# Optimization experiments

Measured on AMD Instinct MI355X. Metric: run time of the kernel, lower is better.

The kernel has to match this reference:

```python
import jax, jax.numpy as jnp
import numpy as np

DIM = 1024
HEADS = 16
HIDDEN = int(DIM * 4.0)


def setup_inputs() -> dict:
    key = jax.random.key(0)
    ks = jax.random.split(key, 12)
    s = 0.02
    return {
        "x": jax.random.normal(ks[0], (16, 1024, DIM), dtype=jnp.float32),
        "ln1_g": jnp.ones((DIM,), jnp.float32),
        "ln1_b": jnp.zeros((DIM,), jnp.float32),
        "w_qkv": jax.random.normal(ks[1], (DIM, 3 * DIM), jnp.float32) * s,
        "b_qkv": jnp.zeros((3 * DIM,), jnp.float32),
        "w_proj": jax.random.normal(ks[2], (DIM, DIM), jnp.float32) * s,
        "b_proj": jnp.zeros((DIM,), jnp.float32),
        "ln2_g": jnp.ones((DIM,), jnp.float32),
        "ln2_b": jnp.zeros((DIM,), jnp.float32),
        "w_fc1": jax.random.normal(ks[3], (DIM, HIDDEN), jnp.float32) * s,
        "b_fc1": jnp.zeros((HIDDEN,), jnp.float32),
        "w_fc2": jax.random.normal(ks[4], (HIDDEN, DIM), jnp.float32) * s,
        "b_fc2": jnp.zeros((DIM,), jnp.float32),
    }


def _layernorm(x, g, b, eps=1e-5):
    mu = jnp.mean(x, axis=-1, keepdims=True)
    var = jnp.var(x, axis=-1, keepdims=True)
    return (x - mu) * jax.lax.rsqrt(var + eps) * g + b


def reference(x, ln1_g, ln1_b, w_qkv, b_qkv, w_proj, b_proj,
              ln2_g, ln2_b, w_fc1, b_fc1, w_fc2, b_fc2):
    B, N, C = x.shape
    H = HEADS
    hd = C // H
    scale = hd ** -0.5

    h = _layernorm(x, ln1_g, ln1_b)
    qkv = h @ w_qkv + b_qkv                      # [B,N,3C]
    qkv = qkv.reshape(B, N, 3, H, hd).transpose(2, 0, 3, 1, 4)
    q, k, v = qkv[0], qkv[1], qkv[2]             # [B,H,N,hd]

    attn = jnp.einsum("bhqd,bhkd->bhqk", q, k) * scale
    # original does explicit max-subtract then softmax; identical to stable softmax
    attn = jax.nn.softmax(attn, axis=-1)
    ctx = jnp.einsum("bhqk,bhkd->bhqd", attn, v)  # [B,H,N,hd]
    ctx = ctx.transpose(0, 2, 1, 3).reshape(B, N, C)
    attn_out = ctx @ w_proj + b_proj

    x = x + attn_out
    h2 = _layernorm(x, ln2_g, ln2_b)
    m = jax.nn.gelu(h2 @ w_fc1 + b_fc1, approximate=False)
    m = m @ w_fc2 + b_fc2
    return x + m
```

## Files before the change

### kernel.cpp

```cpp
#include <hip/hip_runtime.h>
#include <hip/hip_bf16.h>
#include <math.h>

using v8s   = __attribute__((ext_vector_type(8))) short;
using f32x4 = __attribute__((ext_vector_type(4))) float;

#define DEV __device__ __forceinline__

DEV void gload16(const void* g, void* l) {
  __builtin_amdgcn_global_load_lds(
      (const __attribute__((address_space(1))) unsigned int*)g,
      (__attribute__((address_space(3))) unsigned int*)l,
      16, 0, 0);
}

__global__ __launch_bounds__(256) void transpose_cast(
    const float* __restrict__ in, __hip_bfloat16* __restrict__ out, int K, int N)
{
  __shared__ float tile[32][33];
  const int n0 = blockIdx.x * 32, k0 = blockIdx.y * 32;
  const int tx = threadIdx.x, ty = threadIdx.y;
#pragma unroll
  for (int j = 0; j < 4; ++j)
    tile[ty + j*8][tx] = in[(size_t)(k0 + ty + j*8) * N + n0 + tx];
  __syncthreads();
#pragma unroll
  for (int j = 0; j < 4; ++j)
    out[(size_t)(n0 + ty + j*8) * K + k0 + tx] = __float2bfloat16(tile[tx][ty + j*8]);
}

__global__ __launch_bounds__(256) void ln_kernel(
    const float* __restrict__ xin, const float* __restrict__ g,
    const float* __restrict__ b, __hip_bfloat16* __restrict__ outp)
{
  const int row = blockIdx.x;
  const int t = threadIdx.x;
  const float4 v = ((const float4*)(xin + (size_t)row * 1024))[t];
  float s  = v.x + v.y + v.z + v.w;
  float ss = v.x*v.x + v.y*v.y + v.z*v.z + v.w*v.w;
  for (int off = 32; off > 0; off >>= 1) { s += __shfl_down(s, off); ss += __shfl_down(ss, off); }
  __shared__ float red[8];
  const int w = t >> 6;
  if ((t & 63) == 0) { red[w*2] = s; red[w*2 + 1] = ss; }
  __syncthreads();
  s  = red[0] + red[2] + red[4] + red[6];
  ss = red[1] + red[3] + red[5] + red[7];
  const float mu   = s * (1.0f / 1024.0f);
  const float rstd = rsqrtf(ss * (1.0f / 1024.0f) - mu * mu + 1e-5f);
  const float4 gv = ((const float4*)g)[t];
  const float4 bv = ((const float4*)b)[t];
  __hip_bfloat16* o = outp + (size_t)row * 1024 + t * 4;
  o[0] = __float2bfloat16((v.x - mu) * rstd * gv.x + bv.x);
  o[1] = __float2bfloat16((v.y - mu) * rstd * gv.y + bv.y);
  o[2] = __float2bfloat16((v.z - mu) * rstd * gv.z + bv.z);
  o[3] = __float2bfloat16((v.w - mu) * rstd * gv.w + bv.w);
}

#define STAGE_A(tile, ks, buf) do { int tt_ = (tile) < NT ? (tile) : NT - 1;     \
  _Pragma("unroll") for (int rr_ = 0; rr_ < 2; ++rr_) {                          \
    const int c_ = rr_*512 + t; const int row_ = c_ >> 2; const int sl_ = c_ & 3;\
    const int sw_ = sl_ ^ ((row_ >> 1) & 3);                                     \
    gload16(A + (size_t)(bm0 + row_) * K + tt_*64 + (ks)*32 + sw_*8,             \
            &As[buf][ks][row_][sl_*8]); } } while (0)

#define STAGE_B(tile, ks, buf) do { int tt_ = (tile) < NT ? (tile) : NT - 1;     \
  _Pragma("unroll") for (int rr_ = 0; rr_ < 2; ++rr_) {                          \
    const int c_ = rr_*512 + t; const int row_ = c_ >> 2; const int sl_ = c_ & 3;\
    const int sw_ = sl_ ^ ((row_ >> 1) & 3);                                     \
    gload16(Bt + (size_t)(bn0 + row_) * K + tt_*64 + (ks)*32 + sw_*8,            \
            &Bs[buf][ks][row_][sl_*8]); } } while (0)

#define LDB4(dst, c, ks) do { _Pragma("unroll") for (int n_ = 0; n_ < 4; ++n_) { \
  const int row_ = bwrow + n_*16;                                                \
  dst[n_] = *(const v8s*)&Bs[c][ks][row_][(lg ^ ((row_>>1)&3))*8]; } } while (0)

#define LDA4(dst, c, ks, mh) do { _Pragma("unroll") for (int m_ = 0; m_ < 4; ++m_) { \
  const int row_ = awrow + (mh)*64 + m_*16;                                      \
  dst[m_] = *(const v8s*)&As[c][ks][row_][(lg ^ ((row_>>1)&3))*8]; } } while (0)

#define MFMA16(av, bv, mh) do {                                                  \
  __builtin_amdgcn_s_setprio(1);                                                 \
  _Pragma("unroll") for (int mi_ = 0; mi_ < 4; ++mi_)                            \
    _Pragma("unroll") for (int n_ = 0; n_ < 4; ++n_)                             \
      acc[(mh)*4 + mi_][n_] = __builtin_amdgcn_mfma_f32_16x16x32_bf16(           \
          av[mi_], bv[n_], acc[(mh)*4 + mi_][n_], 0, 0, 0);                      \
  __builtin_amdgcn_s_setprio(0); } while (0)

template<int EPI>
__global__ __launch_bounds__(512, 2) void gemm256(
    const __hip_bfloat16* __restrict__ A, const __hip_bfloat16* __restrict__ Bt,
    const float* __restrict__ bias, const float* resid, void* outp,
    __hip_bfloat16* __restrict__ vt, int N, int K, int nbx)
{
  __shared__ __hip_bfloat16 As[2][2][256][32];
  __shared__ __hip_bfloat16 Bs[2][2][256][32];

  const int t = threadIdx.x;
  const int w = t >> 6, l = t & 63;
  const int wm = w >> 2, wn = w & 3;
  const int lr = l & 15, lg = l >> 4;
  const int awrow = wm * 128 + lr;
  const int bwrow = wn * 64 + lr;

  const int cpx  = gridDim.x >> 3;
  const int xcd  = blockIdx.x & 7;
  const int lid  = blockIdx.x >> 3;
  const int nbyc = cpx / nbx;
  const int span = nbyc * 4;
  const int gx   = lid / span;
  const int rem  = lid - gx * span;
  const int by   = xcd * nbyc + (rem >> 2);
  const int bx   = gx * 4 + (rem & 3);
  const size_t bm0 = (size_t)by * 256, bn0 = (size_t)bx * 256;

  const int NT = K >> 6;

  const f32x4 zz = {0.f, 0.f, 0.f, 0.f};
  f32x4 acc[8][4];
#pragma unroll
  for (int i = 0; i < 8; ++i)
#pragma unroll
    for (int j = 0; j < 4; ++j) acc[i][j] = zz;

  STAGE_A(0, 0, 0); STAGE_B(0, 0, 0);
  STAGE_A(0, 1, 0); STAGE_B(0, 1, 0);
  asm volatile("s_waitcnt vmcnt(0)" ::: "memory");
  __builtin_amdgcn_s_barrier();

  for (int tt = 0; tt < NT; ++tt) {
    const int c = tt & 1;
    v8s b0[4], a0[4], a1[4], b1[4], a2[4], a3[4];
    LDB4(b0, c, 0); LDA4(a0, c, 0, 0); LDA4(a1, c, 0, 1);
    LDB4(b1, c, 1); LDA4(a2, c, 1, 0); LDA4(a3, c, 1, 1);
    STAGE_A(tt + 1, 0, c ^ 1); STAGE_B(tt + 1, 0, c ^ 1);
    STAGE_A(tt + 1, 1, c ^ 1); STAGE_B(tt + 1, 1, c ^ 1);
    asm volatile("s_waitcnt lgkmcnt(12)" ::: "memory");
    __builtin_amdgcn_sched_barrier(0);
    MFMA16(a0, b0, 0);
    MFMA16(a1, b0, 1);
    asm volatile("s_waitcnt lgkmcnt(0)" ::: "memory");
    __builtin_amdgcn_sched_barrier(0);
    MFMA16(a2, b1, 0);
    MFMA16(a3, b1, 1);
    asm volatile("s_waitcnt vmcnt(0)" ::: "memory");
    __builtin_amdgcn_s_barrier();
  }

#pragma unroll
  for (int m = 0; m < 8; ++m)
#pragma unroll
    for (int n = 0; n < 4; ++n) {
      const int col = (int)bn0 + wn * 64 + n * 16 + lr;
      const float bz = bias[col];
#pragma unroll
      for (int r = 0; r < 4; ++r) {
        const int row = (int)bm0 + wm * 128 + m * 16 + lg * 4 + r;
        const float v = acc[m][n][r] + bz;
        if (EPI == 1) {
          ((float*)outp)[(size_t)row * N + col] = v + resid[(size_t)row * N + col];
        } else if (EPI == 2) {
          const float gel = 0.5f * v * (1.0f + erff(v * 0.70710678118654752f));
          ((__hip_bfloat16*)outp)[(size_t)row * N + col] = __float2bfloat16(gel);
        } else {
          if (col < 2048) {
            const float vv = (col < 1024) ? v * 0.18033688011112042f : v;
            ((__hip_bfloat16*)outp)[(size_t)row * 3072 + col] = __float2bfloat16(vv);
          } else {
            const int d = col - 2048;
            const int hh = d >> 6, dd = d & 63;
            const int bbq = row >> 10, nn = row & 1023;
            const int nnp = (nn & ~31) | (((nn & 15) << 1) | ((nn >> 4) & 1));
            vt[(((size_t)bbq * 16 + hh) * 64 + dd) * 1024 + nnp] = __float2bfloat16(v);
          }
        }
      }
    }
}

__global__ __launch_bounds__(512) void attn_kernel(
    const __hip_bfloat16* __restrict__ qkv, const __hip_bfloat16* __restrict__ vt,
    __hip_bfloat16* __restrict__ ctx)
{
  __shared__ __hip_bfloat16 Ks[2][64 * 64];
  __shared__ __hip_bfloat16 Vs[2][64 * 64];
  __shared__ __hip_bfloat16 Ps[8][32][72];

  const int t = threadIdx.x;
  const int w = t >> 6, l = t & 63;
  const int lr = l & 15, lg = l >> 4;

  const int lin  = blockIdx.x;
  const int xcd  = lin & 7;
  const int slot = lin >> 3;
  const int head = xcd * 32 + (slot >> 2);
  const int q0   = (slot & 3) * 256;
  const int bb = head >> 4, h = head & 15;
  const int tok0 = bb * 1024;
  const int qrow_base = tok0 + q0 + w * 32;

  const int srow0 = t >> 3, ssl0 = t & 7, ssw0 = ssl0 ^ (srow0 & 7);

  v8s qf[2][2];
#pragma unroll
  for (int i = 0; i < 2; ++i)
#pragma unroll
    for (int k2 = 0; k2 < 2; ++k2)
      qf[i][k2] = *(const v8s*)(qkv + (size_t)(qrow_base + i * 16 + lr) * 3072 + h * 64 + k2 * 32 + lg * 8);

  v8s vone;
#pragma unroll
  for (int e = 0; e < 8; ++e) vone[e] = (short)0x3F80;

  const f32x4 zz = {0.f, 0.f, 0.f, 0.f};
  f32x4 oacc[2][5];
#pragma unroll
  for (int i = 0; i < 2; ++i)
#pragma unroll
    for (int dg = 0; dg < 5; ++dg) oacc[i][dg] = zz;

  {
    gload16(qkv + (size_t)(tok0 + srow0) * 3072 + 1024 + h * 64 + ssw0 * 8, &Ks[0][t * 8]);
    gload16(vt  + (size_t)(head * 64 + srow0) * 1024 + ssw0 * 8,            &Vs[0][t * 8]);
  }
  asm volatile("s_waitcnt vmcnt(0)" ::: "memory");
  __builtin_amdgcn_s_barrier();

  for (int kt = 0; kt < 16; ++kt) {
    const int cur = kt & 1;
    if (kt < 15) {
      const int nxt = cur ^ 1;
      const int kn = (kt + 1) * 64;
      gload16(qkv + (size_t)(tok0 + kn + srow0) * 3072 + 1024 + h * 64 + ssw0 * 8, &Ks[nxt][t * 8]);
      gload16(vt  + (size_t)(head * 64 + srow0) * 1024 + kn + ssw0 * 8,            &Vs[nxt][t * 8]);
    }

    f32x4 s[2][4];
#pragma unroll
    for (int i = 0; i < 2; ++i)
#pragma unroll
      for (int j = 0; j < 4; ++j) s[i][j] = zz;
#pragma unroll
    for (int k2 = 0; k2 < 2; ++k2) {
      v8s kb[4];
#pragma unroll
      for (int j = 0; j < 4; ++j) {
        const int row = j * 16 + lr;
        kb[j] = *(const v8s*)(&Ks[cur][row * 64 + (((k2 * 4 + lg) ^ (row & 7)) * 8)]);
      }
#pragma unroll
      for (int i = 0; i < 2; ++i)
#pragma unroll
        for (int j = 0; j < 4; ++j)
          s[i][j] = __builtin_amdgcn_mfma_f32_16x16x32_bf16(qf[i][k2], kb[j], s[i][j], 0, 0, 0);
    }

#pragma unroll
    for (int i = 0; i < 2; ++i)
#pragma unroll
      for (int jj = 0; jj < 2; ++jj)
#pragma unroll
        for (int r = 0; r < 4; ++r) {
          const float lo = exp2f(s[i][2*jj][r]);
          const float hi = exp2f(s[i][2*jj + 1][r]);
          unsigned int pk;
          asm("v_cvt_pk_bf16_f32 %0, %1, %2" : "=v"(pk) : "v"(lo), "v"(hi));
          *(unsigned int*)&Ps[w][i * 16 + lg * 4 + r][jj * 32 + lr * 2] = pk;
        }

#pragma unroll
    for (int k2 = 0; k2 < 2; ++k2) {
      v8s pa[2];
#pragma unroll
      for (int i = 0; i < 2; ++i)
        pa[i] = *(const v8s*)&Ps[w][i * 16 + lr][k2 * 32 + lg * 8];
#pragma unroll
      for (int dg = 0; dg < 4; ++dg) {
        const int row = dg * 16 + lr;
        v8s vb = *(const v8s*)(&Vs[cur][row * 64 + (((k2 * 4 + lg) ^ (row & 7)) * 8)]);
#pragma unroll
        for (int i = 0; i < 2; ++i)
          oacc[i][dg] = __builtin_amdgcn_mfma_f32_16x16x32_bf16(pa[i], vb, oacc[i][dg], 0, 0, 0);
      }
#pragma unroll
      for (int i = 0; i < 2; ++i)
        oacc[i][4] = __builtin_amdgcn_mfma_f32_16x16x32_bf16(pa[i], vone, oacc[i][4], 0, 0, 0);
    }

    asm volatile("s_waitcnt vmcnt(0)" ::: "memory");
    __builtin_amdgcn_s_barrier();
  }

#pragma unroll
  for (int i = 0; i < 2; ++i) {
    float inv[4];
#pragma unroll
    for (int r = 0; r < 4; ++r) inv[r] = 1.0f / oacc[i][4][r];
#pragma unroll
    for (int dg = 0; dg < 4; ++dg)
#pragma unroll
      for (int r = 0; r < 4; ++r) {
        const int qrow = qrow_base + i * 16 + lg * 4 + r;
        ctx[(size_t)qrow * 1024 + h * 64 + dg * 16 + lr] = __float2bfloat16(oacc[i][dg][r] * inv[r]);
      }
  }
}

extern "C" void kernel_launch(void* const* d_in, const int* in_sizes, int n_in,
                              void* d_out, int out_size, void* d_ws, size_t ws_size,
                              hipStream_t stream) {
  const float* x      = (const float*)d_in[0];
  const float* ln1_g  = (const float*)d_in[1];
  const float* ln1_b  = (const float*)d_in[2];
  const float* w_qkv  = (const float*)d_in[3];
  const float* b_qkv  = (const float*)d_in[4];
  const float* w_proj = (const float*)d_in[5];
  const float* b_proj = (const float*)d_in[6];
  const float* ln2_g  = (const float*)d_in[7];
  const float* ln2_b  = (const float*)d_in[8];
  const float* w_fc1  = (const float*)d_in[9];
  const float* b_fc1  = (const float*)d_in[10];
  const float* w_fc2  = (const float*)d_in[11];
  const float* b_fc2  = (const float*)d_in[12];
  float* out = (float*)d_out;

  char* ws = (char*)d_ws;
  size_t off = 0;
  auto alloc = [&](size_t bytes) { char* p = ws + off; off += bytes; return p; };
  __hip_bfloat16* wqkvt  = (__hip_bfloat16*)alloc((size_t)3072 * 1024 * 2);
  __hip_bfloat16* wprojt = (__hip_bfloat16*)alloc((size_t)1024 * 1024 * 2);
  __hip_bfloat16* wfc1t  = (__hip_bfloat16*)alloc((size_t)4096 * 1024 * 2);
  __hip_bfloat16* wfc2t  = (__hip_bfloat16*)alloc((size_t)1024 * 4096 * 2);
  __hip_bfloat16* h      = (__hip_bfloat16*)alloc((size_t)16384 * 1024 * 2);
  __hip_bfloat16* qkvb   = (__hip_bfloat16*)alloc((size_t)16384 * 3072 * 2);
  __hip_bfloat16* vt     = (__hip_bfloat16*)alloc((size_t)256 * 64 * 1024 * 2);
  __hip_bfloat16* ctx    = (__hip_bfloat16*)alloc((size_t)16384 * 1024 * 2);
  __hip_bfloat16* mbuf   = qkvb;

  transpose_cast<<<dim3(3072/32, 1024/32), dim3(32, 8), 0, stream>>>(w_qkv,  wqkvt,  1024, 3072);
  transpose_cast<<<dim3(1024/32, 1024/32), dim3(32, 8), 0, stream>>>(w_proj, wprojt, 1024, 1024);
  transpose_cast<<<dim3(4096/32, 1024/32), dim3(32, 8), 0, stream>>>(w_fc1,  wfc1t,  1024, 4096);
  transpose_cast<<<dim3(1024/32, 4096/32), dim3(32, 8), 0, stream>>>(w_fc2,  wfc2t,  4096, 1024);

  ln_kernel<<<16384, 256, 0, stream>>>(x, ln1_g, ln1_b, h);
  gemm256<3><<<12 * 64, 512, 0, stream>>>(h,    wqkvt,  b_qkv,  nullptr, qkvb,  vt,      3072, 1024, 12);
  attn_kernel<<<1024, 512, 0, stream>>>(qkvb, vt, ctx);
  gemm256<1><<< 4 * 64, 512, 0, stream>>>(ctx,  wprojt, b_proj, x,       d_out, nullptr, 1024, 1024, 4);
  ln_kernel<<<16384, 256, 0, stream>>>(out, ln2_g, ln2_b, h);
  gemm256<2><<<16 * 64, 512, 0, stream>>>(h,    wfc1t,  b_fc1,  nullptr, mbuf,  nullptr, 4096, 1024, 16);
  gemm256<1><<< 4 * 64, 512, 0, stream>>>(mbuf, wfc2t,  b_fc2,  out,     d_out, nullptr, 1024, 4096, 4);
}
```

Baseline: 773.9 us.

## Replace 256x256 double-buffered GEMM with single-buffered 128x128 tile kernel

Swaps the 512-thread, 256x256-tile, double-buffered GEMM for a 256-thread 128x128-tile kernel with a single LDS buffer per operand, a 64-wide K step, an 8-way XOR swizzle, and a new supertile block mapping across XCDs. Smaller tiles give more blocks (4 per CU by launch bounds) and may improve occupancy and load balance on the small-N projections. In exchange it drops the overlap of global loads with MFMA (load then wait each iteration) and lowers arithmetic intensity per tile, which raises global/L2 traffic.

```diff
diff --git a/kernel.cpp b/kernel.cpp
--- a/kernel.cpp
+++ b/kernel.cpp
@@ -56,105 +56,91 @@
   o[3] = __float2bfloat16((v.w - mu) * rstd * gv.w + bv.w);
 }
 
-#define STAGE_A(tile, ks, buf) do { int tt_ = (tile) < NT ? (tile) : NT - 1;     \
-  _Pragma("unroll") for (int rr_ = 0; rr_ < 2; ++rr_) {                          \
-    const int c_ = rr_*512 + t; const int row_ = c_ >> 2; const int sl_ = c_ & 3;\
-    const int sw_ = sl_ ^ ((row_ >> 1) & 3);                                     \
-    gload16(A + (size_t)(bm0 + row_) * K + tt_*64 + (ks)*32 + sw_*8,             \
-            &As[buf][ks][row_][sl_*8]); } } while (0)
-
-#define STAGE_B(tile, ks, buf) do { int tt_ = (tile) < NT ? (tile) : NT - 1;     \
-  _Pragma("unroll") for (int rr_ = 0; rr_ < 2; ++rr_) {                          \
-    const int c_ = rr_*512 + t; const int row_ = c_ >> 2; const int sl_ = c_ & 3;\
-    const int sw_ = sl_ ^ ((row_ >> 1) & 3);                                     \
-    gload16(Bt + (size_t)(bn0 + row_) * K + tt_*64 + (ks)*32 + sw_*8,            \
-            &Bs[buf][ks][row_][sl_*8]); } } while (0)
-
-#define LDB4(dst, c, ks) do { _Pragma("unroll") for (int n_ = 0; n_ < 4; ++n_) { \
-  const int row_ = bwrow + n_*16;                                                \
-  dst[n_] = *(const v8s*)&Bs[c][ks][row_][(lg ^ ((row_>>1)&3))*8]; } } while (0)
-
-#define LDA4(dst, c, ks, mh) do { _Pragma("unroll") for (int m_ = 0; m_ < 4; ++m_) { \
-  const int row_ = awrow + (mh)*64 + m_*16;                                      \
-  dst[m_] = *(const v8s*)&As[c][ks][row_][(lg ^ ((row_>>1)&3))*8]; } } while (0)
-
-#define MFMA16(av, bv, mh) do {                                                  \
-  __builtin_amdgcn_s_setprio(1);                                                 \
-  _Pragma("unroll") for (int mi_ = 0; mi_ < 4; ++mi_)                            \
-    _Pragma("unroll") for (int n_ = 0; n_ < 4; ++n_)                             \
-      acc[(mh)*4 + mi_][n_] = __builtin_amdgcn_mfma_f32_16x16x32_bf16(           \
-          av[mi_], bv[n_], acc[(mh)*4 + mi_][n_], 0, 0, 0);                      \
-  __builtin_amdgcn_s_setprio(0); } while (0)
+
+#define STAGE_T(tile) do { const int tt_ = (tile);                               \
+  _Pragma("unroll") for (int rr_ = 0; rr_ < 4; ++rr_) {                          \
+    const int c_ = rr_*256 + t; const int row_ = c_ >> 3; const int sl_ = c_ & 7;\
+    const int sw_ = sl_ ^ (row_ & 7);                                            \
+    gload16(A + (size_t)(bm0 + row_) * K + tt_*64 + sw_*8, &As[row_][sl_*8]); }  \
+  _Pragma("unroll") for (int rr_ = 0; rr_ < 4; ++rr_) {                          \
+    const int c_ = rr_*256 + t; const int row_ = c_ >> 3; const int sl_ = c_ & 7;\
+    const int sw_ = sl_ ^ (row_ & 7);                                            \
+    gload16(Bt + (size_t)(bn0 + row_) * K + tt_*64 + sw_*8, &Bs[row_][sl_*8]); } } while (0)
+
+#define LDAB(k2) do {                                                            \
+  _Pragma("unroll") for (int mi_ = 0; mi_ < 4; ++mi_) {                          \
+    const int r_ = wm*64 + mi_*16 + lr;                                          \
+    a_[mi_] = *(const v8s*)&As[r_][((((k2)*4)+lg) ^ (r_ & 7))*8]; }              \
+  _Pragma("unroll") for (int ni_ = 0; ni_ < 4; ++ni_) {                          \
+    const int r_ = wn*64 + ni_*16 + lr;                                          \
+    b_[ni_] = *(const v8s*)&Bs[r_][((((k2)*4)+lg) ^ (r_ & 7))*8]; } } while (0)
 
 template<int EPI>
-__global__ __launch_bounds__(512, 2) void gemm256(
+__global__ __launch_bounds__(256, 4) void gemm128(
     const __hip_bfloat16* __restrict__ A, const __hip_bfloat16* __restrict__ Bt,
     const float* __restrict__ bias, const float* resid, void* outp,
     __hip_bfloat16* __restrict__ vt, int N, int K, int nbx)
 {
-  __shared__ __hip_bfloat16 As[2][2][256][32];
-  __shared__ __hip_bfloat16 Bs[2][2][256][32];
+  __shared__ __hip_bfloat16 As[128][64];
+  __shared__ __hip_bfloat16 Bs[128][64];
 
   const int t = threadIdx.x;
   const int w = t >> 6, l = t & 63;
-  const int wm = w >> 2, wn = w & 3;
+  const int wm = w >> 1, wn = w & 1;
   const int lr = l & 15, lg = l >> 4;
-  const int awrow = wm * 128 + lr;
-  const int bwrow = wn * 64 + lr;
-
-  const int cpx  = gridDim.x >> 3;
+
   const int xcd  = blockIdx.x & 7;
   const int lid  = blockIdx.x >> 3;
-  const int nbyc = cpx / nbx;
-  const int span = nbyc * 4;
-  const int gx   = lid / span;
-  const int rem  = lid - gx * span;
-  const int by   = xcd * nbyc + (rem >> 2);
-  const int bx   = gx * 4 + (rem & 3);
-  const size_t bm0 = (size_t)by * 256, bn0 = (size_t)bx * 256;
+  const int super = lid >> 5;
+  const int rem   = lid & 31;
+  const int nsx   = nbx >> 2;
+  const int gy    = super / nsx;
+  const int gx    = super - gy * nsx;
+  const int by    = xcd * 16 + gy * 8 + (rem >> 2);
+  const int bx    = gx * 4 + (rem & 3);
+  const size_t bm0 = (size_t)by * 128, bn0 = (size_t)bx * 128;
 
   const int NT = K >> 6;
 
   const f32x4 zz = {0.f, 0.f, 0.f, 0.f};
-  f32x4 acc[8][4];
-#pragma unroll
-  for (int i = 0; i < 8; ++i)
+  f32x4 acc[4][4];
+#pragma unroll
+  for (int i = 0; i < 4; ++i)
 #pragma unroll
     for (int j = 0; j < 4; ++j) acc[i][j] = zz;
 
-  STAGE_A(0, 0, 0); STAGE_B(0, 0, 0);
-  STAGE_A(0, 1, 0); STAGE_B(0, 1, 0);
-  asm volatile("s_waitcnt vmcnt(0)" ::: "memory");
-  __builtin_amdgcn_s_barrier();
-
+  v8s a_[4], b_[4];
   for (int tt = 0; tt < NT; ++tt) {
-    const int c = tt & 1;
-    v8s b0[4], a0[4], a1[4], b1[4], a2[4], a3[4];
-    LDB4(b0, c, 0); LDA4(a0, c, 0, 0); LDA4(a1, c, 0, 1);
-    LDB4(b1, c, 1); LDA4(a2, c, 1, 0); LDA4(a3, c, 1, 1);
-    STAGE_A(tt + 1, 0, c ^ 1); STAGE_B(tt + 1, 0, c ^ 1);
-    STAGE_A(tt + 1, 1, c ^ 1); STAGE_B(tt + 1, 1, c ^ 1);
-    asm volatile("s_waitcnt lgkmcnt(12)" ::: "memory");
-    __builtin_amdgcn_sched_barrier(0);
-    MFMA16(a0, b0, 0);
-    MFMA16(a1, b0, 1);
-    asm volatile("s_waitcnt lgkmcnt(0)" ::: "memory");
-    __builtin_amdgcn_sched_barrier(0);
-    MFMA16(a2, b1, 0);
-    MFMA16(a3, b1, 1);
+    STAGE_T(tt);
     asm volatile("s_waitcnt vmcnt(0)" ::: "memory");
     __builtin_amdgcn_s_barrier();
+    __builtin_amdgcn_sched_barrier(0);
+#pragma unroll
+    for (int k2 = 0; k2 < 2; ++k2) {
+      LDAB(k2);
+      asm volatile("s_waitcnt lgkmcnt(0)" ::: "memory");
+      __builtin_amdgcn_sched_barrier(0);
+      __builtin_amdgcn_s_setprio(1);
+#pragma unroll
+      for (int mi = 0; mi < 4; ++mi)
+#pragma unroll
+        for (int ni = 0; ni < 4; ++ni)
+          acc[mi][ni] = __builtin_amdgcn_mfma_f32_16x16x32_bf16(a_[mi], b_[ni], acc[mi][ni], 0, 0, 0);
+      __builtin_amdgcn_s_setprio(0);
+    }
+    __builtin_amdgcn_s_barrier();
+    __builtin_amdgcn_sched_barrier(0);
   }
 
 #pragma unroll
-  for (int m = 0; m < 8; ++m)
+  for (int m = 0; m < 4; ++m)
 #pragma unroll
     for (int n = 0; n < 4; ++n) {
       const int col = (int)bn0 + wn * 64 + n * 16 + lr;
       const float bz = bias[col];
 #pragma unroll
       for (int r = 0; r < 4; ++r) {
-        const int row = (int)bm0 + wm * 128 + m * 16 + lg * 4 + r;
+        const int row = (int)bm0 + wm * 64 + m * 16 + lg * 4 + r;
         const float v = acc[m][n][r] + bz;
         if (EPI == 1) {
           ((float*)outp)[(size_t)row * N + col] = v + resid[(size_t)row * N + col];
@@ -342,10 +328,10 @@
   transpose_cast<<<dim3(1024/32, 4096/32), dim3(32, 8), 0, stream>>>(w_fc2,  wfc2t,  4096, 1024);
 
   ln_kernel<<<16384, 256, 0, stream>>>(x, ln1_g, ln1_b, h);
-  gemm256<3><<<12 * 64, 512, 0, stream>>>(h,    wqkvt,  b_qkv,  nullptr, qkvb,  vt,      3072, 1024, 12);
+  gemm128<3><<<16 * 24 * 8, 256, 0, stream>>>(h,    wqkvt,  b_qkv,  nullptr, qkvb,  vt,      3072, 1024, 24);
   attn_kernel<<<1024, 512, 0, stream>>>(qkvb, vt, ctx);
-  gemm256<1><<< 4 * 64, 512, 0, stream>>>(ctx,  wprojt, b_proj, x,       d_out, nullptr, 1024, 1024, 4);
+  gemm128<1><<<16 *  8 * 8, 256, 0, stream>>>(ctx,  wprojt, b_proj, x,       d_out, nullptr, 1024, 1024, 8);
   ln_kernel<<<16384, 256, 0, stream>>>(out, ln2_g, ln2_b, h);
-  gemm256<2><<<16 * 64, 512, 0, stream>>>(h,    wfc1t,  b_fc1,  nullptr, mbuf,  nullptr, 4096, 1024, 16);
-  gemm256<1><<< 4 * 64, 512, 0, stream>>>(mbuf, wfc2t,  b_fc2,  out,     d_out, nullptr, 1024, 4096, 4);
-}
+  gemm128<2><<<16 * 32 * 8, 256, 0, stream>>>(h,    wfc1t,  b_fc1,  nullptr, mbuf,  nullptr, 4096, 1024, 32);
+  gemm128<1><<<16 *  8 * 8, 256, 0, stream>>>(mbuf, wfc2t,  b_fc2,  out,     d_out, nullptr, 1024, 4096, 8);
+}
```

Result: faster. 703.4 us (median of 3 runs) (-9.1%).

## Restructure GEMM mainloop into 8-phase quadrant pipeline with half-tile staging

Applied to the files above, without the earlier changes.

Reorganizes the bf16 GEMM shared-memory layout from two 32-wide k-slices into two 128-row halves of 64-wide k, with an 8-way XOR swizzle. The main loop becomes eight phases per pair of k-tiles. Each phase loads one quadrant of A/B fragments, issues one half-tile global-to-LDS stage and runs 16 MFMAs between barriers, so loads stay in flight across phases (vmcnt(2)). The intent is finer-grained overlap of global loads, LDS reads and MFMA work. It adds many more barriers per tile and assumes NT is even.

```diff
diff --git a/kernel.cpp b/kernel.cpp
--- a/kernel.cpp
+++ b/kernel.cpp
@@ -56,35 +56,50 @@
   o[3] = __float2bfloat16((v.w - mu) * rstd * gv.w + bv.w);
 }
 
-#define STAGE_A(tile, ks, buf) do { int tt_ = (tile) < NT ? (tile) : NT - 1;     \
+
+#define STAGE_AH(T, h, bf) do { int tt_ = (T) < NT ? (T) : NT - 1;               \
   _Pragma("unroll") for (int rr_ = 0; rr_ < 2; ++rr_) {                          \
-    const int c_ = rr_*512 + t; const int row_ = c_ >> 2; const int sl_ = c_ & 3;\
-    const int sw_ = sl_ ^ ((row_ >> 1) & 3);                                     \
-    gload16(A + (size_t)(bm0 + row_) * K + tt_*64 + (ks)*32 + sw_*8,             \
-            &As[buf][ks][row_][sl_*8]); } } while (0)
-
-#define STAGE_B(tile, ks, buf) do { int tt_ = (tile) < NT ? (tile) : NT - 1;     \
+    const int c_ = rr_*512 + t; const int row_ = c_ >> 3; const int sl_ = c_ & 7;\
+    const int sw_ = sl_ ^ (row_ & 7);                                            \
+    gload16(A + (size_t)(bm0 + (h)*128 + row_) * K + tt_*64 + sw_*8,             \
+            &As[bf][h][row_][sl_*8]); } } while (0)
+
+#define STAGE_BH(T, h, bf) do { int tt_ = (T) < NT ? (T) : NT - 1;               \
   _Pragma("unroll") for (int rr_ = 0; rr_ < 2; ++rr_) {                          \
-    const int c_ = rr_*512 + t; const int row_ = c_ >> 2; const int sl_ = c_ & 3;\
-    const int sw_ = sl_ ^ ((row_ >> 1) & 3);                                     \
-    gload16(Bt + (size_t)(bn0 + row_) * K + tt_*64 + (ks)*32 + sw_*8,            \
-            &Bs[buf][ks][row_][sl_*8]); } } while (0)
-
-#define LDB4(dst, c, ks) do { _Pragma("unroll") for (int n_ = 0; n_ < 4; ++n_) { \
-  const int row_ = bwrow + n_*16;                                                \
-  dst[n_] = *(const v8s*)&Bs[c][ks][row_][(lg ^ ((row_>>1)&3))*8]; } } while (0)
-
-#define LDA4(dst, c, ks, mh) do { _Pragma("unroll") for (int m_ = 0; m_ < 4; ++m_) { \
-  const int row_ = awrow + (mh)*64 + m_*16;                                      \
-  dst[m_] = *(const v8s*)&As[c][ks][row_][(lg ^ ((row_>>1)&3))*8]; } } while (0)
-
-#define MFMA16(av, bv, mh) do {                                                  \
+    const int c_ = rr_*512 + t; const int row_ = c_ >> 3; const int sl_ = c_ & 7;\
+    const int sw_ = sl_ ^ (row_ & 7);                                            \
+    gload16(Bt + (size_t)(bn0 + (h)*128 + row_) * K + tt_*64 + sw_*8,            \
+            &Bs[bf][h][row_][sl_*8]); } } while (0)
+
+#define LDAQ(bf, mq) do { _Pragma("unroll") for (int ks_ = 0; ks_ < 2; ++ks_)    \
+  _Pragma("unroll") for (int mi_ = 0; mi_ < 4; ++mi_) {                          \
+    const int r_ = (mq)*64 + mi_*16 + lr;                                        \
+    a_[ks_][mi_] = *(const v8s*)&As[bf][wm][r_][((ks_*4 + lg) ^ (r_ & 7))*8]; } } while (0)
+
+#define LDBQ(bf, nq) do { _Pragma("unroll") for (int ks_ = 0; ks_ < 2; ++ks_)    \
+  _Pragma("unroll") for (int ni_ = 0; ni_ < 2; ++ni_) {                          \
+    const int r_ = (wn & 1)*64 + (nq)*32 + ni_*16 + lr;                          \
+    b_[ks_][ni_] = *(const v8s*)&Bs[bf][wn>>1][r_][((ks_*4 + lg) ^ (r_ & 7))*8]; } } while (0)
+
+#define PHASE_Q(bf, mq, nq, FA, FB, STAGE_STMT, VMC) do {                        \
+  if (FA) LDAQ(bf, mq);                                                          \
+  if (FB) LDBQ(bf, nq);                                                          \
+  STAGE_STMT;                                                                    \
+  __builtin_amdgcn_s_barrier();                                                  \
+  __builtin_amdgcn_sched_barrier(0);                                             \
+  asm volatile("s_waitcnt lgkmcnt(0)" ::: "memory");                             \
+  __builtin_amdgcn_sched_barrier(0);                                             \
   __builtin_amdgcn_s_setprio(1);                                                 \
   _Pragma("unroll") for (int mi_ = 0; mi_ < 4; ++mi_)                            \
-    _Pragma("unroll") for (int n_ = 0; n_ < 4; ++n_)                             \
-      acc[(mh)*4 + mi_][n_] = __builtin_amdgcn_mfma_f32_16x16x32_bf16(           \
-          av[mi_], bv[n_], acc[(mh)*4 + mi_][n_], 0, 0, 0);                      \
-  __builtin_amdgcn_s_setprio(0); } while (0)
+    _Pragma("unroll") for (int ni_ = 0; ni_ < 2; ++ni_)                          \
+      _Pragma("unroll") for (int ks_ = 0; ks_ < 2; ++ks_)                        \
+        acc[(mq)*4 + mi_][(nq)*2 + ni_] = __builtin_amdgcn_mfma_f32_16x16x32_bf16( \
+            a_[ks_][mi_], b_[ks_][ni_], acc[(mq)*4 + mi_][(nq)*2 + ni_], 0, 0, 0); \
+  __builtin_amdgcn_s_setprio(0);                                                 \
+  if (VMC) asm volatile("s_waitcnt vmcnt(2)" ::: "memory");                      \
+  __builtin_amdgcn_s_barrier();                                                  \
+  __builtin_amdgcn_sched_barrier(0);                                             \
+} while (0)
 
 template<int EPI>
 __global__ __launch_bounds__(512, 2) void gemm256(
@@ -92,15 +107,13 @@
     const float* __restrict__ bias, const float* resid, void* outp,
     __hip_bfloat16* __restrict__ vt, int N, int K, int nbx)
 {
-  __shared__ __hip_bfloat16 As[2][2][256][32];
-  __shared__ __hip_bfloat16 Bs[2][2][256][32];
+  __shared__ __hip_bfloat16 As[2][2][128][64];
+  __shared__ __hip_bfloat16 Bs[2][2][128][64];
 
   const int t = threadIdx.x;
   const int w = t >> 6, l = t & 63;
   const int wm = w >> 2, wn = w & 3;
   const int lr = l & 15, lg = l >> 4;
-  const int awrow = wm * 128 + lr;
-  const int bwrow = wn * 64 + lr;
 
   const int cpx  = gridDim.x >> 3;
   const int xcd  = blockIdx.x & 7;
@@ -122,28 +135,24 @@
 #pragma unroll
     for (int j = 0; j < 4; ++j) acc[i][j] = zz;
 
-  STAGE_A(0, 0, 0); STAGE_B(0, 0, 0);
-  STAGE_A(0, 1, 0); STAGE_B(0, 1, 0);
-  asm volatile("s_waitcnt vmcnt(0)" ::: "memory");
+  STAGE_AH(0, 0, 0); STAGE_BH(0, 0, 0); STAGE_AH(0, 1, 0); STAGE_BH(0, 1, 0);
+  STAGE_AH(1, 0, 1);
+  asm volatile("s_waitcnt vmcnt(2)" ::: "memory");
   __builtin_amdgcn_s_barrier();
-
-  for (int tt = 0; tt < NT; ++tt) {
-    const int c = tt & 1;
-    v8s b0[4], a0[4], a1[4], b1[4], a2[4], a3[4];
-    LDB4(b0, c, 0); LDA4(a0, c, 0, 0); LDA4(a1, c, 0, 1);
-    LDB4(b1, c, 1); LDA4(a2, c, 1, 0); LDA4(a3, c, 1, 1);
-    STAGE_A(tt + 1, 0, c ^ 1); STAGE_B(tt + 1, 0, c ^ 1);
-    STAGE_A(tt + 1, 1, c ^ 1); STAGE_B(tt + 1, 1, c ^ 1);
-    asm volatile("s_waitcnt lgkmcnt(12)" ::: "memory");
-    __builtin_amdgcn_sched_barrier(0);
-    MFMA16(a0, b0, 0);
-    MFMA16(a1, b0, 1);
-    asm volatile("s_waitcnt lgkmcnt(0)" ::: "memory");
-    __builtin_amdgcn_sched_barrier(0);
-    MFMA16(a2, b1, 0);
-    MFMA16(a3, b1, 1);
-    asm volatile("s_waitcnt vmcnt(0)" ::: "memory");
-    __builtin_amdgcn_s_barrier();
+  __builtin_amdgcn_sched_barrier(0);
+
+  v8s a_[2][4], b_[2][2];
+  const int NI = NT >> 1;
+  for (int i = 0; i < NI; ++i) {
+    const int E = 2 * i;
+    PHASE_Q(0, 0, 0, 1, 1, STAGE_AH(E + 1, 1, 1), 0);
+    PHASE_Q(0, 0, 1, 0, 1, STAGE_BH(E + 1, 0, 1), 0);
+    PHASE_Q(0, 1, 1, 1, 0, STAGE_BH(E + 1, 1, 1), 0);
+    PHASE_Q(0, 1, 0, 0, 1, STAGE_AH(E + 2, 0, 0), 1);
+    PHASE_Q(1, 0, 0, 1, 1, STAGE_AH(E + 2, 1, 0), 0);
+    PHASE_Q(1, 0, 1, 0, 1, STAGE_BH(E + 2, 0, 0), 0);
+    PHASE_Q(1, 1, 1, 1, 0, STAGE_BH(E + 2, 1, 0), 0);
+    PHASE_Q(1, 1, 0, 0, 1, STAGE_AH(E + 3, 0, 1), 1);
   }
 
 #pragma unroll
```

Result: slower. 818.7 us (+5.8%).
